# Optimization experiments

Hardware: AMD Instinct MI355X
Metric: run time of the kernel (lower is better)

The kernel has to match this reference:

```python
import jax, jax.numpy as jnp
import numpy as np

N = 100000
E = 3200000
F_IN, H1, H2, C = 128, 64, 32, 10


def setup_inputs() -> dict:
    key = jax.random.key(0)
    ks = jax.random.split(key, 8)
    x = jax.random.normal(ks[0], (N, F_IN), dtype=jnp.float32)
    edge_index = jax.random.randint(ks[1], (2, E), 0, N, dtype=jnp.int64)
    W1 = jax.random.normal(ks[2], (F_IN, H1), dtype=jnp.float32) / np.sqrt(F_IN)
    b1 = jnp.zeros((H1,), dtype=jnp.float32)
    W2 = jax.random.normal(ks[3], (H1, H2), dtype=jnp.float32) / np.sqrt(H1)
    b2 = jnp.zeros((H2,), dtype=jnp.float32)
    Wc = jax.random.normal(ks[4], (H2, C), dtype=jnp.float32) / np.sqrt(H2)
    bc = jnp.zeros((C,), dtype=jnp.float32)
    return {"x": x, "edge_index": edge_index, "W1": W1, "b1": b1,
            "W2": W2, "b2": b2, "Wc": Wc, "bc": bc}


def gcn_conv(x, src, dst, W, b, n):
    # PyG GCNConv: x' = D^{-1/2} (A + I) D^{-1/2} (X W) + b
    h = x @ W                                        # [N, H]
    ones = jnp.ones((src.shape[0],), dtype=h.dtype)
    deg = jax.ops.segment_sum(ones, dst, num_segments=n) + 1.0  # +1 self loop
    dinv = jax.lax.rsqrt(deg)                        # deg >= 1, safe
    norm = dinv[src] * dinv[dst]                     # [E]
    msg = h[src] * norm[:, None]                     # [E, H] gather + scale
    agg = jax.ops.segment_sum(msg, dst, num_segments=n)
    # self-loop contribution: norm_ii = 1/deg_i
    out = agg + h * (dinv * dinv)[:, None]
    return out + b


def reference(x, edge_index, W1, b1, W2, b2, Wc, bc):
    n = x.shape[0]
    src, dst = edge_index[0], edge_index[1]
    h = gcn_conv(x, src, dst, W1, b1, n)
    h = jax.nn.relu(h)
    # dropout is identity in eval mode (training=False)
    h = gcn_conv(h, src, dst, W2, b2, n)
    h = jax.nn.relu(h)
    logits = h @ Wc + bc
    return jax.nn.log_softmax(logits, axis=1)
```

## Files before the change

### kernel.cpp

```cpp
#include <hip/hip_runtime.h>


#define BSHIFT 8
#define BMASK 255
#define NBUCK_MAX 512
#define TILE 4096
#define EPT 16
#define NPW 4

__device__ __forceinline__ unsigned pack_bf16(float lo, float hi) {
    unsigned ul = __float_as_uint(lo);
    ul = (ul + 0x7FFFu + ((ul >> 16) & 1u)) >> 16;
    unsigned uh = __float_as_uint(hi);
    uh = ((uh + 0x7FFFu + ((uh >> 16) & 1u)) >> 16) << 16;
    return ul | uh;
}

__global__ void k_hist(const int* __restrict__ dst, int* __restrict__ bcnt, int E) {
    __shared__ int h[NBUCK_MAX];
    for (int i = threadIdx.x; i < NBUCK_MAX; i += blockDim.x) h[i] = 0;
    __syncthreads();
    for (int e = blockIdx.x * blockDim.x + threadIdx.x; e < E; e += gridDim.x * blockDim.x)
        atomicAdd(&h[dst[e] >> BSHIFT], 1);
    __syncthreads();
    for (int i = threadIdx.x; i < NBUCK_MAX; i += blockDim.x)
        if (h[i]) atomicAdd(&bcnt[i], h[i]);
}

__global__ void k_scanb(const int* __restrict__ bcnt, int* __restrict__ bbase,
                        int* __restrict__ gcur, int E) {
    __shared__ int s[NBUCK_MAX];
    int t = threadIdx.x;
    int v = bcnt[t];
    s[t] = v;
    __syncthreads();
    for (int o = 1; o < NBUCK_MAX; o <<= 1) {
        int u = (t >= o) ? s[t - o] : 0;
        __syncthreads();
        s[t] += u;
        __syncthreads();
    }
    int ex = s[t] - v;
    bbase[t] = ex;
    gcur[t] = ex;
    if (t == NBUCK_MAX - 1) bbase[NBUCK_MAX] = E;
}

__global__ __launch_bounds__(256) void k_binA(const int* __restrict__ src,
                                              const int* __restrict__ dst,
                                              int* __restrict__ gcur,
                                              int* __restrict__ binned, int E) {
    __shared__ int hist[NBUCK_MAX];
    __shared__ int lbase[NBUCK_MAX];
    __shared__ int gdelta[NBUCK_MAX];
    __shared__ int cnt2[NBUCK_MAX];
    __shared__ int scanb[256];
    __shared__ int stage[TILE];
    __shared__ unsigned short sbucket[TILE];

    int t = threadIdx.x;
    for (int i = t; i < NBUCK_MAX; i += 256) { hist[i] = 0; cnt2[i] = 0; }
    __syncthreads();

    int tileStart = blockIdx.x * TILE;
    int cntTile = min(TILE, E - tileStart);

    int vals[EPT];
    int bks[EPT];
#pragma unroll
    for (int i = 0; i < EPT; i++) {
        int e = tileStart + t + i * 256;
        if (e < E) {
            int s = src[e], d = dst[e];
            vals[i] = s | ((d & BMASK) << 17);
            bks[i] = d >> BSHIFT;
            atomicAdd(&hist[bks[i]], 1);
        } else bks[i] = -1;
    }
    __syncthreads();

    int a0 = hist[2 * t], a1 = hist[2 * t + 1];
    int ts = a0 + a1;
    scanb[t] = ts;
    __syncthreads();
    for (int o = 1; o < 256; o <<= 1) {
        int u = (t >= o) ? scanb[t - o] : 0;
        __syncthreads();
        scanb[t] += u;
        __syncthreads();
    }
    int ex = scanb[t] - ts;
    lbase[2 * t] = ex;
    lbase[2 * t + 1] = ex + a0;
    __syncthreads();

    for (int b = t; b < NBUCK_MAX; b += 256) {
        int c = hist[b];
        int g = c ? atomicAdd(&gcur[b], c) : 0;
        gdelta[b] = g - lbase[b];
    }
#pragma unroll
    for (int i = 0; i < EPT; i++) {
        if (bks[i] >= 0) {
            int rr = atomicAdd(&cnt2[bks[i]], 1);
            int slot = lbase[bks[i]] + rr;
            stage[slot] = vals[i];
            sbucket[slot] = (unsigned short)bks[i];
        }
    }
    __syncthreads();
    for (int i = t; i < cntTile; i += 256) {
        int b = sbucket[i];
        binned[gdelta[b] + i] = stage[i];
    }
}

__global__ void k_sortcsr(const int* __restrict__ bbase, const int* __restrict__ binned,
                          int* __restrict__ rowptr, float* __restrict__ dinv,
                          int* __restrict__ csr, int n, int E) {
    __shared__ int cnt[256];
    __shared__ int sc[256];
    __shared__ int rpl[256];
    __shared__ int lcur[256];
    int b = blockIdx.x, t = threadIdx.x;
    cnt[t] = 0; lcur[t] = 0;
    __syncthreads();
    int beg = bbase[b], end = bbase[b + 1];
    for (int i = beg + t; i < end; i += 256)
        atomicAdd(&cnt[(binned[i] >> 17) & BMASK], 1);
    __syncthreads();
    int v = cnt[t];
    sc[t] = v;
    __syncthreads();
    for (int o = 1; o < 256; o <<= 1) {
        int u = (t >= o) ? sc[t - o] : 0;
        __syncthreads();
        sc[t] += u;
        __syncthreads();
    }
    int rp = beg + sc[t] - v;
    rpl[t] = rp;
    int g = (b << BSHIFT) + t;
    if (g < n) {
        rowptr[g] = rp;
        dinv[g] = rsqrtf((float)v + 1.0f);
        if (g == n - 1) rowptr[n] = E;
    }
    __syncthreads();
    for (int i = beg + t; i < end; i += 256) {
        int vv = binned[i];
        int ln = (vv >> 17) & BMASK;
        int k = atomicAdd(&lcur[ln], 1);
        csr[rpl[ln] + k] = vv & 0x1FFFF;
    }
}

template<int K, int M, int R>
__global__ __launch_bounds__(256) void k_gemm(const float* __restrict__ X,
                                              const float* __restrict__ W,
                                              const float* __restrict__ dinv,
                                              unsigned* __restrict__ hsb, int n) {
    constexpr int MW = M / 4;
    __shared__ float Ws[K * M];
    for (int i = threadIdx.x; i < K * M; i += 256) Ws[i] = W[i];
    __syncthreads();
    int w = threadIdx.x >> 6, lane = threadIdx.x & 63;
    int wo = w * MW;
    int r0 = blockIdx.x * (64 * R) + lane;
    float acc[R][MW];
#pragma unroll
    for (int i = 0; i < R; i++)
#pragma unroll
        for (int j = 0; j < MW; j++) acc[i][j] = 0.f;

    for (int k = 0; k < K; k += 4) {
        float4 xv[R];
#pragma unroll
        for (int i = 0; i < R; i++) {
            int rr = r0 + 64 * i;
            xv[i] = (rr < n) ? *(const float4*)(X + (size_t)rr * K + k)
                             : make_float4(0.f, 0.f, 0.f, 0.f);
        }
#pragma unroll
        for (int kk = 0; kk < 4; kk++) {
#pragma unroll
            for (int j = 0; j < MW; j += 4) {
                float4 wv = *(const float4*)&Ws[(k + kk) * M + wo + j];
#pragma unroll
                for (int i = 0; i < R; i++) {
                    float xs = (kk == 0) ? xv[i].x : (kk == 1) ? xv[i].y
                             : (kk == 2) ? xv[i].z : xv[i].w;
                    acc[i][j + 0] += xs * wv.x;
                    acc[i][j + 1] += xs * wv.y;
                    acc[i][j + 2] += xs * wv.z;
                    acc[i][j + 3] += xs * wv.w;
                }
            }
        }
    }
#pragma unroll
    for (int i = 0; i < R; i++) {
        int rr = r0 + 64 * i;
        if (rr < n) {
            float di = dinv[rr];
            unsigned p[MW / 2];
#pragma unroll
            for (int jj = 0; jj < MW / 2; jj++)
                p[jj] = pack_bf16(acc[i][2 * jj] * di, acc[i][2 * jj + 1] * di);
            unsigned* hr = hsb + (size_t)rr * (M / 2) + wo / 2;
#pragma unroll
            for (int jj = 0; jj < MW / 2; jj += 4)
                *(uint4*)(hr + jj) = make_uint4(p[jj], p[jj + 1], p[jj + 2], p[jj + 3]);
        }
    }
}

#define ACC8(V) \
    acc[0] += __uint_as_float((V).x << 16);  acc[1] += __uint_as_float((V).x & 0xFFFF0000u); \
    acc[2] += __uint_as_float((V).y << 16);  acc[3] += __uint_as_float((V).y & 0xFFFF0000u); \
    acc[4] += __uint_as_float((V).z << 16);  acc[5] += __uint_as_float((V).z & 0xFFFF0000u); \
    acc[6] += __uint_as_float((V).w << 16);  acc[7] += __uint_as_float((V).w & 0xFFFF0000u);

__global__ __launch_bounds__(256) void k_agg64f(
        const int* __restrict__ rowptr, const int* __restrict__ csr,
        const uint4* __restrict__ hsb, const float* __restrict__ dinv,
        const float* __restrict__ b1, const float* __restrict__ W2,
        unsigned* __restrict__ hsb2, int n) {
    int wid = (blockIdx.x * blockDim.x + threadIdx.x) >> 6;
    int lane = threadIdx.x & 63;
    int q = lane >> 3, r = lane & 7;
    int d0 = wid * NPW;
    if (d0 >= n) return;
    float w2r[8][4];
    float b1r[8];
#pragma unroll
    for (int i = 0; i < 8; i++) {
        b1r[i] = b1[8 * r + i];
#pragma unroll
        for (int jj = 0; jj < 4; jj++)
            w2r[i][jj] = W2[(8 * r + i) * 32 + 4 * q + jj];
    }
    int dend = min(d0 + NPW, n);
    for (int d = d0; d < dend; d++) {
        int beg = rowptr[d], end = rowptr[d + 1];
        float acc[8];
#pragma unroll
        for (int i = 0; i < 8; i++) acc[i] = 0.f;
        int base = beg;
        for (; base + 16 <= end; base += 16) {
            int sA = csr[base + q];
            int sB = csr[base + 8 + q];
            uint4 wA = hsb[(size_t)sA * 8 + r];
            uint4 wB = hsb[(size_t)sB * 8 + r];
            ACC8(wA)
            ACC8(wB)
        }
        if (base + q < end) {
            uint4 wv = hsb[(size_t)csr[base + q] * 8 + r];
            ACC8(wv)
        }
        if (base + 8 + q < end) {
            uint4 wv = hsb[(size_t)csr[base + 8 + q] * 8 + r];
            ACC8(wv)
        }
#pragma unroll
        for (int i = 0; i < 8; i++) {
            acc[i] += __shfl_xor(acc[i], 8, 64);
            acc[i] += __shfl_xor(acc[i], 16, 64);
            acc[i] += __shfl_xor(acc[i], 32, 64);
        }
        uint4 wsf = hsb[(size_t)d * 8 + r];
        ACC8(wsf)
        float di = dinv[d];
        float v[8];
#pragma unroll
        for (int i = 0; i < 8; i++) v[i] = fmaxf(acc[i] * di + b1r[i], 0.f);
        float h[4] = {0.f, 0.f, 0.f, 0.f};
#pragma unroll
        for (int i = 0; i < 8; i++)
#pragma unroll
            for (int jj = 0; jj < 4; jj++) h[jj] += v[i] * w2r[i][jj];
#pragma unroll
        for (int jj = 0; jj < 4; jj++) {
            h[jj] += __shfl_xor(h[jj], 1, 64);
            h[jj] += __shfl_xor(h[jj], 2, 64);
            h[jj] += __shfl_xor(h[jj], 4, 64);
        }
        if (r == 0) {
            unsigned p0 = pack_bf16(h[0] * di, h[1] * di);
            unsigned p1 = pack_bf16(h[2] * di, h[3] * di);
            *(uint2*)(hsb2 + (size_t)d * 16 + 2 * q) = make_uint2(p0, p1);
        }
    }
}

__global__ __launch_bounds__(256) void k_agg32f(
        const int* __restrict__ rowptr, const int* __restrict__ csr,
        const uint4* __restrict__ hsb2, const float* __restrict__ dinv,
        const float* __restrict__ b2, const float* __restrict__ Wc,
        const float* __restrict__ bc, float* __restrict__ out, int n) {
    int wid = (blockIdx.x * blockDim.x + threadIdx.x) >> 6;
    int lane = threadIdx.x & 63;
    int q = lane >> 2, r = lane & 3;
    int d0 = wid * NPW;
    if (d0 >= n) return;
    float wcr[8];
    float b2r[8];
    float bcr = (q < 10) ? bc[q] : 0.f;
#pragma unroll
    for (int i = 0; i < 8; i++) {
        b2r[i] = b2[8 * r + i];
        wcr[i] = (q < 10) ? Wc[(8 * r + i) * 10 + q] : 0.f;
    }
    int dend = min(d0 + NPW, n);
    for (int d = d0; d < dend; d++) {
        int beg = rowptr[d], end = rowptr[d + 1];
        float acc[8];
#pragma unroll
        for (int i = 0; i < 8; i++) acc[i] = 0.f;
        int base = beg;
        for (; base + 32 <= end; base += 32) {
            int sA = csr[base + q];
            int sB = csr[base + 16 + q];
            uint4 wA = hsb2[(size_t)sA * 4 + r];
            uint4 wB = hsb2[(size_t)sB * 4 + r];
            ACC8(wA)
            ACC8(wB)
        }
        if (base + q < end) {
            uint4 wv = hsb2[(size_t)csr[base + q] * 4 + r];
            ACC8(wv)
        }
        if (base + 16 + q < end) {
            uint4 wv = hsb2[(size_t)csr[base + 16 + q] * 4 + r];
            ACC8(wv)
        }
#pragma unroll
        for (int i = 0; i < 8; i++) {
            acc[i] += __shfl_xor(acc[i], 4, 64);
            acc[i] += __shfl_xor(acc[i], 8, 64);
            acc[i] += __shfl_xor(acc[i], 16, 64);
            acc[i] += __shfl_xor(acc[i], 32, 64);
        }
        uint4 wsf = hsb2[(size_t)d * 4 + r];
        ACC8(wsf)
        float di = dinv[d];
        float part = 0.f;
#pragma unroll
        for (int i = 0; i < 8; i++) {
            float v = fmaxf(acc[i] * di + b2r[i], 0.f);
            part += v * wcr[i];
        }
        part += __shfl_xor(part, 1, 64);
        part += __shfl_xor(part, 2, 64);
        float mylogit = part + bcr;
        float m = -1e30f;
        float l[10];
#pragma unroll
        for (int c = 0; c < 10; c++) {
            l[c] = __shfl(mylogit, 4 * c, 64);
            m = fmaxf(m, l[c]);
        }
        float ssum = 0.f;
#pragma unroll
        for (int c = 0; c < 10; c++) ssum += __expf(l[c] - m);
        float lse = m + __logf(ssum);
        if (r == 0 && q < 10) out[(size_t)d * 10 + q] = mylogit - lse;
    }
}

extern "C" void kernel_launch(void* const* d_in, const int* in_sizes, int n_in,
                              void* d_out, int out_size, void* d_ws, size_t ws_size,
                              hipStream_t stream) {
    const float* x  = (const float*)d_in[0];
    const int*   ei = (const int*)d_in[1];
    const float* W1 = (const float*)d_in[2];
    const float* b1 = (const float*)d_in[3];
    const float* W2 = (const float*)d_in[4];
    const float* b2 = (const float*)d_in[5];
    const float* Wc = (const float*)d_in[6];
    const float* bc = (const float*)d_in[7];
    float* out = (float*)d_out;

    const int N = in_sizes[0] / 128;
    const int E = in_sizes[1] / 2;
    const int* src = ei;
    const int* dst = ei + E;

    const int NBUCK = (N + BMASK) >> BSHIFT;
    const int NTILE = (E + TILE - 1) / TILE;
    const int NW = (N + NPW - 1) / NPW;

    char* ws = (char*)d_ws;
    size_t off = 0;
    auto alloc = [&](size_t elems) {
        void* p = ws + off;
        off += ((elems * 4 + 1023) & ~(size_t)1023);
        return p;
    };
    float*    dinv   = (float*)alloc(N);
    int*      bcnt   = (int*)alloc(NBUCK_MAX);
    int*      bbase  = (int*)alloc(NBUCK_MAX + 1);
    int*      gcur   = (int*)alloc(NBUCK_MAX);
    int*      rowptr = (int*)alloc(N + 1);
    int*      binned = (int*)alloc(E);
    int*      csr    = (int*)alloc(E);
    unsigned* hsb    = (unsigned*)alloc((size_t)N * 32);
    unsigned* hsb2   = (unsigned*)alloc((size_t)N * 16);

    hipMemsetAsync(bcnt, 0, sizeof(int) * NBUCK_MAX, stream);

    k_hist<<<512, 256, 0, stream>>>(dst, bcnt, E);
    k_scanb<<<1, NBUCK_MAX, 0, stream>>>(bcnt, bbase, gcur, E);
    k_binA<<<NTILE, 256, 0, stream>>>(src, dst, gcur, binned, E);
    k_sortcsr<<<NBUCK, 256, 0, stream>>>(bbase, binned, rowptr, dinv, csr, N, E);

    k_gemm<128, 64, 2><<<(N + 127) / 128, 256, 0, stream>>>(x, W1, dinv, hsb, N);
    k_agg64f<<<(NW * 64 + 255) / 256, 256, 0, stream>>>(rowptr, csr, (const uint4*)hsb,
                                                        dinv, b1, W2, hsb2, N);
    k_agg32f<<<(NW * 64 + 255) / 256, 256, 0, stream>>>(rowptr, csr, (const uint4*)hsb2,
                                                        dinv, b2, Wc, bc, out, N);
}
```

Baseline: 364.9 us.

## Preload neighbor indices per row into registers and software-pipeline gathers

In both aggregation kernels, each wave now loads up to 64 CSR neighbor indices with one coalesced read and hands them out through lane shuffles, instead of re-reading csr for every gather. The feature gathers are double-buffered so the next pair of loads is in flight while the current pair accumulates. The next row's rowptr and index block are prefetched during the current row's reductions, and the self-loop row and dinv are loaded early. Rows with more than 64 neighbors fall back to direct csr reads. The cost is extra register pressure and shuffle instructions.

```diff
diff --git a/kernel.cpp b/kernel.cpp
--- a/kernel.cpp
+++ b/kernel.cpp
@@ -241,27 +241,46 @@
             w2r[i][jj] = W2[(8 * r + i) * 32 + 4 * q + jj];
     }
     int dend = min(d0 + NPW, n);
+    int beg = rowptr[d0];
+    int end = rowptr[d0 + 1];
+    int cc = min(end - beg, 64);
+    int idxv = (lane < cc) ? csr[beg + lane] : 0;
     for (int d = d0; d < dend; d++) {
-        int beg = rowptr[d], end = rowptr[d + 1];
+        uint4 wsf = hsb[(size_t)d * 8 + r];
+        float di = dinv[d];
         float acc[8];
 #pragma unroll
         for (int i = 0; i < 8; i++) acc[i] = 0.f;
-        int base = beg;
-        for (; base + 16 <= end; base += 16) {
-            int sA = csr[base + q];
-            int sB = csr[base + 8 + q];
-            uint4 wA = hsb[(size_t)sA * 8 + r];
-            uint4 wB = hsb[(size_t)sB * 8 + r];
+        int j = 0;
+        if (cc >= 16) {
+            uint4 wA = hsb[(size_t)__shfl(idxv, q, 64) * 8 + r];
+            uint4 wB = hsb[(size_t)__shfl(idxv, 8 + q, 64) * 8 + r];
+            for (j = 16; j + 16 <= cc; j += 16) {
+                uint4 nA = hsb[(size_t)__shfl(idxv, j + q, 64) * 8 + r];
+                uint4 nB = hsb[(size_t)__shfl(idxv, j + 8 + q, 64) * 8 + r];
+                ACC8(wA)
+                ACC8(wB)
+                wA = nA; wB = nB;
+            }
             ACC8(wA)
             ACC8(wB)
         }
-        if (base + q < end) {
-            uint4 wv = hsb[(size_t)csr[base + q] * 8 + r];
-            ACC8(wv)
-        }
-        if (base + 8 + q < end) {
-            uint4 wv = hsb[(size_t)csr[base + 8 + q] * 8 + r];
-            ACC8(wv)
+        {
+            int tA = j + q, tB = j + 8 + q;
+            int sA = __shfl(idxv, tA & 63, 64);
+            int sB = __shfl(idxv, tB & 63, 64);
+            if (tA < cc) { uint4 wv = hsb[(size_t)sA * 8 + r]; ACC8(wv) }
+            if (tB < cc) { uint4 wv = hsb[(size_t)sB * 8 + r]; ACC8(wv) }
+        }
+        for (int c = beg + 64; c < end; c += 16) {
+            if (c + q < end)     { uint4 wv = hsb[(size_t)csr[c + q] * 8 + r]; ACC8(wv) }
+            if (c + 8 + q < end) { uint4 wv = hsb[(size_t)csr[c + 8 + q] * 8 + r]; ACC8(wv) }
+        }
+        int nbeg = 0, nend = 0, ncc = 0, nidxv = 0;
+        if (d + 1 < dend) {
+            nbeg = end; nend = rowptr[d + 2];
+            ncc = min(nend - nbeg, 64);
+            nidxv = (lane < ncc) ? csr[nbeg + lane] : 0;
         }
 #pragma unroll
         for (int i = 0; i < 8; i++) {
@@ -269,9 +288,7 @@
             acc[i] += __shfl_xor(acc[i], 16, 64);
             acc[i] += __shfl_xor(acc[i], 32, 64);
         }
-        uint4 wsf = hsb[(size_t)d * 8 + r];
         ACC8(wsf)
-        float di = dinv[d];
         float v[8];
 #pragma unroll
         for (int i = 0; i < 8; i++) v[i] = fmaxf(acc[i] * di + b1r[i], 0.f);
@@ -291,6 +308,7 @@
             unsigned p1 = pack_bf16(h[2] * di, h[3] * di);
             *(uint2*)(hsb2 + (size_t)d * 16 + 2 * q) = make_uint2(p0, p1);
         }
+        beg = nbeg; end = nend; cc = ncc; idxv = nidxv;
     }
 }
 
@@ -313,27 +331,46 @@
         wcr[i] = (q < 10) ? Wc[(8 * r + i) * 10 + q] : 0.f;
     }
     int dend = min(d0 + NPW, n);
+    int beg = rowptr[d0];
+    int end = rowptr[d0 + 1];
+    int cc = min(end - beg, 64);
+    int idxv = (lane < cc) ? csr[beg + lane] : 0;
     for (int d = d0; d < dend; d++) {
-        int beg = rowptr[d], end = rowptr[d + 1];
+        uint4 wsf = hsb2[(size_t)d * 4 + r];
+        float di = dinv[d];
         float acc[8];
 #pragma unroll
         for (int i = 0; i < 8; i++) acc[i] = 0.f;
-        int base = beg;
-        for (; base + 32 <= end; base += 32) {
-            int sA = csr[base + q];
-            int sB = csr[base + 16 + q];
-            uint4 wA = hsb2[(size_t)sA * 4 + r];
-            uint4 wB = hsb2[(size_t)sB * 4 + r];
+        int j = 0;
+        if (cc >= 32) {
+            uint4 wA = hsb2[(size_t)__shfl(idxv, q, 64) * 4 + r];
+            uint4 wB = hsb2[(size_t)__shfl(idxv, 16 + q, 64) * 4 + r];
+            for (j = 32; j + 32 <= cc; j += 32) {
+                uint4 nA = hsb2[(size_t)__shfl(idxv, j + q, 64) * 4 + r];
+                uint4 nB = hsb2[(size_t)__shfl(idxv, j + 16 + q, 64) * 4 + r];
+                ACC8(wA)
+                ACC8(wB)
+                wA = nA; wB = nB;
+            }
             ACC8(wA)
             ACC8(wB)
         }
-        if (base + q < end) {
-            uint4 wv = hsb2[(size_t)csr[base + q] * 4 + r];
-            ACC8(wv)
-        }
-        if (base + 16 + q < end) {
-            uint4 wv = hsb2[(size_t)csr[base + 16 + q] * 4 + r];
-            ACC8(wv)
+        {
+            int tA = j + q, tB = j + 16 + q;
+            int sA = __shfl(idxv, tA & 63, 64);
+            int sB = __shfl(idxv, tB & 63, 64);
+            if (tA < cc) { uint4 wv = hsb2[(size_t)sA * 4 + r]; ACC8(wv) }
+            if (tB < cc) { uint4 wv = hsb2[(size_t)sB * 4 + r]; ACC8(wv) }
+        }
+        for (int c = beg + 64; c < end; c += 32) {
+            if (c + q < end)      { uint4 wv = hsb2[(size_t)csr[c + q] * 4 + r]; ACC8(wv) }
+            if (c + 16 + q < end) { uint4 wv = hsb2[(size_t)csr[c + 16 + q] * 4 + r]; ACC8(wv) }
+        }
+        int nbeg = 0, nend = 0, ncc = 0, nidxv = 0;
+        if (d + 1 < dend) {
+            nbeg = end; nend = rowptr[d + 2];
+            ncc = min(nend - nbeg, 64);
+            nidxv = (lane < ncc) ? csr[nbeg + lane] : 0;
         }
 #pragma unroll
         for (int i = 0; i < 8; i++) {
@@ -342,9 +379,7 @@
             acc[i] += __shfl_xor(acc[i], 16, 64);
             acc[i] += __shfl_xor(acc[i], 32, 64);
         }
-        uint4 wsf = hsb2[(size_t)d * 4 + r];
         ACC8(wsf)
-        float di = dinv[d];
         float part = 0.f;
 #pragma unroll
         for (int i = 0; i < 8; i++) {
@@ -366,6 +401,7 @@
         for (int c = 0; c < 10; c++) ssum += __expf(l[c] - m);
         float lse = m + __logf(ssum);
         if (r == 0 && q < 10) out[(size_t)d * 10 + q] = mylogit - lse;
+        beg = nbeg; end = nend; cc = ncc; idxv = nidxv;
     }
 }
 
```

Result: slower. 372.5 us (+2.1%).
